# Performance work log

Measured on AMD Instinct MI355X. Metric: run time of the kernel, lower is better.

Reference implementation:

```python
import jax, jax.numpy as jnp
import numpy as np

B, T, H, W = 8, 10, 128, 128
WIDTH, NL = 64, 4
MT, MH, MW = 4, 8, 8
H_PRED = 5
MIN_STD = 1e-4


def setup_inputs() -> dict:
    key = jax.random.key(0)
    ks = jax.random.split(key, 12)
    scale = 1.0 / (WIDTH * WIDTH)
    return {
        "frames": jax.random.uniform(ks[0], (B, T, H, W), dtype=jnp.float32),
        "times": jax.random.uniform(ks[1], (B, T), dtype=jnp.float32),
        # lift: Conv3d(c_in=2 -> width, k=1)
        "lift_w": jax.random.normal(ks[2], (WIDTH, 2), dtype=jnp.float32) * 0.5,
        "lift_b": jnp.zeros((WIDTH,), jnp.float32),
        # spectral weights: (layer, quadrant, in, out, mt, mh, mw, re/im)
        "spec_w": jax.random.uniform(ks[3], (NL, 4, WIDTH, WIDTH, MT, MH, MW, 2), dtype=jnp.float32) * scale,
        # skip 1x1 Conv3d per layer
        "skip_w": jax.random.normal(ks[4], (NL, WIDTH, WIDTH), dtype=jnp.float32) * (1.0 / np.sqrt(WIDTH)),
        "skip_b": jnp.zeros((NL, WIDTH), jnp.float32),
        # temporal aggregation Conv3d kernel (h_ctx,1,1): (out, in, T)
        "agg_w": jax.random.normal(ks[5], (WIDTH, WIDTH, T), dtype=jnp.float32) * (1.0 / np.sqrt(WIDTH * T)),
        "agg_b": jnp.zeros((WIDTH,), jnp.float32),
        "fc1_w": jax.random.normal(ks[6], (WIDTH + 2, 128), dtype=jnp.float32) * (1.0 / np.sqrt(WIDTH + 2)),
        "fc1_b": jnp.zeros((128,), jnp.float32),
        "fc2_w": jax.random.normal(ks[7], (128, 2 * H_PRED), dtype=jnp.float32) * (1.0 / np.sqrt(128)),
        "fc2_b": jnp.zeros((2 * H_PRED,), jnp.float32),
    }


def _spectral_conv(x, wl):
    # x: (B, C, T, H, W); wl: (4, C, C, MT, MH, MW, 2) real/imag
    w = wl[..., 0] + 1j * wl[..., 1]  # (4, C, C, MT, MH, MW) complex
    x_ft = jnp.fft.rfftn(x, axes=(-3, -2, -1), norm="ortho")  # (B,C,T,H,W//2+1)
    Bc, C, Tt, Hh, Wf = x_ft.shape

    def mul(blk, wq):
        return jnp.einsum("bixyz,ioxyz->boxyz", blk, wq)

    out_ft = jnp.zeros((Bc, C, Tt, Hh, Wf), dtype=x_ft.dtype)
    out_ft = out_ft.at[:, :, :MT, :MH, :MW].set(mul(x_ft[:, :, :MT, :MH, :MW], w[0]))
    out_ft = out_ft.at[:, :, :MT, Hh - MH:, :MW].set(mul(x_ft[:, :, :MT, Hh - MH:, :MW], w[1]))
    out_ft = out_ft.at[:, :, Tt - MT:, :MH, :MW].set(mul(x_ft[:, :, Tt - MT:, :MH, :MW], w[2]))
    out_ft = out_ft.at[:, :, Tt - MT:, Hh - MH:, :MW].set(mul(x_ft[:, :, Tt - MT:, Hh - MH:, :MW], w[3]))
    return jnp.fft.irfftn(out_ft, s=(Tt, x.shape[-2], x.shape[-1]), axes=(-3, -2, -1), norm="ortho")


def reference(frames, times, lift_w, lift_b, spec_w, skip_w, skip_b,
              agg_w, agg_b, fc1_w, fc1_b, fc2_w, fc2_b):
    gelu = lambda v: jax.nn.gelu(v, approximate=False)
    # feature volume: (B, 2, T, H, W) = [frames, broadcast times]
    t_feat = jnp.broadcast_to(times[:, None, :, None, None], (B, 1, T, H, W))
    feat = jnp.concatenate([frames[:, None], t_feat], axis=1)
    # lift (1x1x1 conv)
    x = jnp.einsum("bcthw,oc->bothw", feat, lift_w) + lift_b[None, :, None, None, None]
    for l in range(NL):
        sx = _spectral_conv(x, spec_w[l])
        sk = jnp.einsum("bithw,oi->bothw", x, skip_w[l]) + skip_b[l][None, :, None, None, None]
        x = gelu(sx + sk)
    # temporal aggregation: valid conv over full T -> (B, C, H, W)
    x = jnp.einsum("bithw,oit->bohw", x, agg_w) + agg_b[None, :, None, None]
    # (x, y) grid channels
    gx = jnp.broadcast_to(jnp.linspace(-1.0, 1.0, W)[None, :], (H, W))
    gy = jnp.broadcast_to(jnp.linspace(-1.0, 1.0, H)[:, None], (H, W))
    grid = jnp.broadcast_to(jnp.stack([gx, gy], 0)[None], (B, 2, H, W))
    x = jnp.concatenate([x, grid], axis=1)  # (B, C+2, H, W)
    x = jnp.transpose(x, (0, 2, 3, 1))      # (B, H, W, C+2)
    x = gelu(x @ fc1_w + fc1_b)
    out = x @ fc2_w + fc2_b                 # (B, H, W, 2*h_pred)
    mu = out[..., 0::2]
    sigma = jax.nn.softplus(out[..., 1::2]) + MIN_STD
    return jnp.concatenate([mu, sigma], axis=-1)  # (B, H, W, 2*h_pred)
```

## Files before the change

kernel.cpp:

```cpp
#include <hip/hip_runtime.h>
#include <math.h>


#define TWO_PI 6.2831853071795864769f
#define ORTHO_SC 2.4705294220065465e-3f

typedef unsigned short u16;
typedef _Float16 f16;
typedef __attribute__((ext_vector_type(8))) _Float16 f16x8;
typedef __attribute__((ext_vector_type(4))) float f32x4;

#define MFMAH(acc, a, b) acc = __builtin_amdgcn_mfma_f32_16x16x32_f16(a, b, acc, 0, 0, 0)

__device__ __forceinline__ u16 f16b(float v) {
  f16 h = (f16)v;
  return __builtin_bit_cast(u16, h);
}
__device__ __forceinline__ float f16lo(float v) {
  f16 h = (f16)v;
  return v - (float)h;
}
__device__ __forceinline__ float f16f(u16 b) {
  return (float)__builtin_bit_cast(f16, b);
}
__device__ __forceinline__ float gelu_fast(float x) {
  float u = 0.7978845608f * (x + 0.044715f * x * x * x);
  float a = fminf(u * 2.885390082f, 30.0f);
  float e = __builtin_exp2f(a);
  return x * e * __builtin_amdgcn_rcpf(e + 1.0f);
}

__global__ __launch_bounds__(256) void k_prep2(const float* __restrict__ skip_w,
                                               const float* __restrict__ agg_w,
                                               u16* __restrict__ swf,
                                               u16* __restrict__ awf,
                                               u16* __restrict__ Tt,
                                               float2* __restrict__ twf,
                                               u16* __restrict__ Ef) {
  int e = blockIdx.x*256 + threadIdx.x;
  if (e < 32768) {
    int j = e & 7, lane = (e >> 3) & 63, half = (e >> 9) & 1, ks = (e >> 10) & 1;
    int strip = (e >> 11) & 3, layer = e >> 13;
    int co = strip*16 + (lane & 15);
    int ci = ks*32 + (lane >> 4)*8 + j;
    float v = skip_w[((size_t)(layer*64) + co)*64 + ci];
    swf[e] = half ? f16b(f16lo(v)) : f16b(v);
  } else if (e < 114688) {
    int ee = e - 32768;
    int j = ee & 7, lane = (ee >> 3) & 63;
    int v9 = ee >> 9;
    int half = v9 & 1; v9 >>= 1;
    int ks = v9 & 1; v9 >>= 1;
    int t = v9 % 10, strip = v9 / 10;
    int co = strip*16 + (lane & 15);
    int ci = ks*32 + (lane >> 4)*8 + j;
    float v = agg_w[((size_t)co*64 + ci)*10 + t];
    awf[ee] = half ? f16b(f16lo(v)) : f16b(v);
  } else if (e < 122880) {
    int ee = e - 114688;
    int half = ee >> 12, r = ee & 4095, w = r >> 5, kk = r & 31;
    int m = kk >> 1;
    float val;
    if (kk >= 16) val = 0.f;
    else if (kk == 0) val = 1.f;
    else if (kk == 1) val = 0.f;
    else {
      float th = TWO_PI * (float)m * (float)w / 128.0f;
      val = (kk & 1) ? (-2.f*sinf(th)) : (2.f*cosf(th));
    }
    Tt[ee] = half ? f16b(f16lo(val)) : f16b(val);
  } else if (e < 123904) {
    int ee = e - 122880;
    int w = ee >> 3, k = ee & 7;
    float th = TWO_PI * (float)k * (float)w / 128.0f;
    twf[ee] = make_float2(cosf(th), -sinf(th));
  } else if (e < 125952) {
    int ee = e - 123904;
    int j = ee & 7, lane = (ee >> 3) & 63, kc = ee >> 9;
    int n = lane & 15, g = lane >> 4;
    int w = kc*32 + g*8 + j;
    int k = n >> 1;
    float th = TWO_PI * (float)k * (float)w / 128.0f;
    float val = (n & 1) ? (-sinf(th)) : cosf(th);
    Ef[ee] = f16b(val);
    Ef[2048 + ee] = f16b(f16lo(val));
  }
}

__global__ __launch_bounds__(128) void k_lift_fwdW(const float* __restrict__ frames,
                                                   const float* __restrict__ times,
                                                   const float* __restrict__ lift_w,
                                                   const float* __restrict__ lift_b,
                                                   const float2* __restrict__ twf,
                                                   u16* __restrict__ xT,
                                                   float* __restrict__ xw) {
  __shared__ u16 xs[64][130];
  __shared__ float2 tws[128][8];
  __shared__ float fr[128];
  __shared__ float lw0[64], lw1a[64];
  int bth = blockIdx.x;
  int h = bth & 127; int bt = bth >> 7; int t = bt % 10, b = bt / 10;
  int tid = threadIdx.x;
  for (int i = tid; i < 1024; i += 128) tws[i >> 3][i & 7] = twf[i];
  float tv = times[b*10 + t];
  fr[tid] = frames[((size_t)(b*10 + t)*128 + h)*128 + tid];
  if (tid < 64) { lw0[tid] = lift_w[2*tid]; lw1a[tid] = lift_w[2*tid+1]*tv + lift_b[tid]; }
  __syncthreads();
  {
    int w = tid;
    float f = fr[w];
    unsigned pk[32];
    #pragma unroll
    for (int q = 0; q < 32; ++q) {
      float v0 = f*lw0[2*q] + lw1a[2*q];
      float v1 = f*lw0[2*q+1] + lw1a[2*q+1];
      u16 h0 = f16b(v0), h1 = f16b(v1);
      xs[2*q][w] = h0; xs[2*q+1][w] = h1;
      pk[q] = (unsigned)h0 | ((unsigned)h1 << 16);
    }
    uint4* d4 = (uint4*)(xT + (size_t)bth*8192 + w*64);
    #pragma unroll
    for (int q = 0; q < 8; ++q)
      d4[q] = make_uint4(pk[4*q], pk[4*q+1], pk[4*q+2], pk[4*q+3]);
  }
  __syncthreads();
  {
    int lane = tid & 63, wv = tid >> 6;
    float ar[4] = {0,0,0,0}, ai[4] = {0,0,0,0};
    for (int w2 = 0; w2 < 128; ++w2) {
      float xu = f16f(xs[lane][w2]);
      #pragma unroll
      for (int kk = 0; kk < 4; ++kk) {
        float2 ew = tws[w2][wv*4 + kk];
        ar[kk] += xu*ew.x; ai[kk] += xu*ew.y;
      }
    }
    size_t row = ((size_t)(b*64 + lane)*10 + t)*128 + h;
    float4* dst = (float4*)(xw + row*16 + wv*8);
    dst[0] = make_float4(ar[0], ai[0], ar[1], ai[1]);
    dst[1] = make_float4(ar[2], ai[2], ar[3], ai[3]);
  }
}

__global__ __launch_bounds__(256) void k_fwdHT(const float2* __restrict__ xw,
                                               float2* __restrict__ xf) {
  __shared__ float2 tile[2][1024];
  __shared__ float2 tw128[128];
  int bc = blockIdx.x;
  int b = bc >> 6, c = bc & 63;
  int tid = threadIdx.x;
  if (tid < 128) {
    float s, co; sincosf(TWO_PI * (float)tid / 128.0f, &s, &co);
    tw128[tid] = make_float2(co, -s);
  }
  int tpar = tid >> 7, j = tid & 127;
  int khi = j >> 3, kwi = j & 7;
  int kh = (khi < 8) ? khi : (112 + khi);
  float accr[8], acci[8];
  #pragma unroll
  for (int k = 0; k < 8; ++k) { accr[k] = 0.f; acci[k] = 0.f; }
  for (int tt = 0; tt < 5; ++tt) {
    __syncthreads();
    for (int u = tid; u < 2048; u += 256) {
      int tg = u >> 10, idx = u & 1023;
      tile[tg][idx] = xw[((size_t)bc*10 + tg*5 + tt)*1024 + idx];
    }
    __syncthreads();
    float xr = 0.f, xi = 0.f;
    for (int h = 0; h < 128; ++h) {
      float2 v = tile[tpar][h*8 + kwi];
      float2 tw = tw128[(h*kh) & 127];
      xr += v.x*tw.x - v.y*tw.y;
      xi += v.x*tw.y + v.y*tw.x;
    }
    int t = tpar*5 + tt;
    float sb, cb; sincosf(TWO_PI * (float)t / 10.0f, &sb, &cb);
    float p_r[10], p_i[10];
    p_r[0] = 1.f; p_i[0] = 0.f; p_r[1] = cb; p_i[1] = -sb;
    #pragma unroll
    for (int k = 2; k < 10; ++k) {
      p_r[k] = p_r[k-1]*p_r[1] - p_i[k-1]*p_i[1];
      p_i[k] = p_r[k-1]*p_i[1] + p_i[k-1]*p_r[1];
    }
    #pragma unroll
    for (int kti = 0; kti < 8; ++kti) {
      int kt = (kti < 4) ? kti : kti + 2;
      accr[kti] += xr*p_r[kt] - xi*p_i[kt];
      acci[kti] += xr*p_i[kt] + xi*p_r[kt];
    }
  }
  __syncthreads();
  float2* parts = &tile[0][0];
  #pragma unroll
  for (int kti = 0; kti < 8; ++kti)
    parts[tpar*1024 + j*8 + kti] = make_float2(accr[kti], acci[kti]);
  __syncthreads();
  if (tpar == 0) {
    #pragma unroll
    for (int kti = 0; kti < 8; ++kti) {
      float2 a = parts[j*8 + kti], bq = parts[1024 + j*8 + kti];
      xf[((size_t)b*1024 + kti*128 + j)*64 + c] =
          make_float2((a.x + bq.x)*ORTHO_SC, (a.y + bq.y)*ORTHO_SC);
    }
  }
}

__global__ __launch_bounds__(256) void k_prep_w4(const float* __restrict__ spec_w,
                                                 float2* __restrict__ wT4) {
  __shared__ float2 tile[64][65];
  int blk = blockIdx.x;
  int l = blk >> 10;
  int inner = blk & 1023;
  int mc = inner & 3, ci = (inner >> 2) & 63, q = inner >> 8;
  const float2* in = (const float2*)spec_w + (size_t)l*4194304
                     + (((size_t)q*64 + ci)*64)*256 + mc*64;
  for (int i = threadIdx.x; i < 4096; i += 256) {
    int co = i >> 6, mm = i & 63;
    tile[co][mm] = in[(size_t)co*256 + mm];
  }
  __syncthreads();
  float2* out = wT4 + (size_t)l*4194304 + ((size_t)q*256 + mc*64)*4096 + (size_t)ci*64;
  for (int i = threadIdx.x; i < 4096; i += 256) {
    int mm = i >> 6, co = i & 63;
    out[(size_t)mm*4096 + co] = tile[co][mm];
  }
}

__global__ __launch_bounds__(256) void k_mix(const float2* __restrict__ xf,
                                             const float2* __restrict__ wTl,
                                             float2* __restrict__ yf) {
  __shared__ float2 xfs[8][4][64];
  int m0 = blockIdx.x * 4;
  for (int i = threadIdx.x; i < 2048; i += 256) {
    int bb = i >> 8, mi = (i >> 6) & 3, ci = i & 63;
    xfs[bb][mi][ci] = xf[((size_t)bb*1024 + m0 + mi)*64 + ci];
  }
  __syncthreads();
  int co = threadIdx.x & 63, mi = threadIdx.x >> 6;
  int m = m0 + mi;
  int kti = m >> 7, khi = (m >> 3) & 15, kwi = m & 7;
  int q = ((kti >= 4) ? 2 : 0) + ((khi >= 8) ? 1 : 0);
  int modeidx = ((kti & 3)*8 + (khi & 7))*8 + kwi;
  const float2* wp = wTl + ((size_t)q*256 + modeidx)*4096 + co;
  float accr[8], acci[8];
  #pragma unroll
  for (int bb = 0; bb < 8; ++bb) { accr[bb] = 0.f; acci[bb] = 0.f; }
  for (int ci = 0; ci < 64; ++ci) {
    float2 wv = wp[(size_t)ci*64];
    #pragma unroll
    for (int bb = 0; bb < 8; ++bb) {
      float2 xv = xfs[bb][mi][ci];
      accr[bb] += xv.x*wv.x - xv.y*wv.y;
      acci[bb] += xv.x*wv.y + xv.y*wv.x;
    }
  }
  #pragma unroll
  for (int bb = 0; bb < 8; ++bb)
    yf[((size_t)bb*64 + co)*1024 + m] = make_float2(accr[bb], acci[bb]);
}

__global__ __launch_bounds__(256) void k_invTH(const float2* __restrict__ yf,
                                               unsigned* __restrict__ zh16) {
  __shared__ float2 ybuf[1024];
  __shared__ float2 ztb[2][128];
  __shared__ float2 tw128[128];
  int bc = blockIdx.x;
  int b = bc >> 6, c = bc & 63;
  int tid = threadIdx.x;
  for (int u = tid; u < 1024; u += 256) ybuf[u] = yf[(size_t)bc*1024 + u];
  if (tid < 128) {
    float s, co; sincosf(TWO_PI * (float)tid / 128.0f, &s, &co);
    tw128[tid] = make_float2(co, s);
  }
  int tpar = tid >> 7, j = tid & 127;
  __syncthreads();
  for (int tt = 0; tt < 5; ++tt) {
    int t = tt*2 + tpar;
    {
      float sb, cb; sincosf(TWO_PI * (float)t / 10.0f, &sb, &cb);
      float p_r[10], p_i[10];
      p_r[0] = 1.f; p_i[0] = 0.f; p_r[1] = cb; p_i[1] = sb;
      #pragma unroll
      for (int k = 2; k < 10; ++k) {
        p_r[k] = p_r[k-1]*p_r[1] - p_i[k-1]*p_i[1];
        p_i[k] = p_r[k-1]*p_i[1] + p_i[k-1]*p_r[1];
      }
      float zr = 0.f, zi = 0.f;
      #pragma unroll
      for (int kti = 0; kti < 8; ++kti) {
        int kt = (kti < 4) ? kti : kti + 2;
        float2 v = ybuf[kti*128 + j];
        zr += v.x*p_r[kt] - v.y*p_i[kt];
        zi += v.x*p_i[kt] + v.y*p_r[kt];
      }
      ztb[tpar][j] = make_float2(zr*ORTHO_SC, zi*ORTHO_SC);
    }
    __syncthreads();
    {
      int h = j;
      float ar[8], ai[8];
      #pragma unroll
      for (int kw = 0; kw < 8; ++kw) { ar[kw] = 0.f; ai[kw] = 0.f; }
      #pragma unroll
      for (int khi = 0; khi < 16; ++khi) {
        int kh = (khi < 8) ? khi : (112 + khi);
        float2 tw = tw128[(h*kh) & 127];
        #pragma unroll
        for (int kw = 0; kw < 8; ++kw) {
          float2 v = ztb[tpar][khi*8 + kw];
          ar[kw] += v.x*tw.x - v.y*tw.y;
          ai[kw] += v.x*tw.y + v.y*tw.x;
        }
      }
      unsigned* dst = zh16 + (((size_t)(b*10 + t)*128 + h)*64 + c)*8;
      #pragma unroll
      for (int kw = 0; kw < 8; ++kw)
        dst[kw] = (unsigned)f16b(ar[kw]) | ((unsigned)f16b(ai[kw]) << 16);
    }
    __syncthreads();
  }
}

__global__ __launch_bounds__(256) void k_invW_mfma(const u16* __restrict__ xTin,
                                                   const unsigned* __restrict__ zh16,
                                                   const u16* __restrict__ swf_l,
                                                   const u16* __restrict__ Tt,
                                                   const u16* __restrict__ Ef,
                                                   const float* __restrict__ skb,
                                                   u16* __restrict__ xTo,
                                                   float* __restrict__ xw,
                                                   int do_dft) {
  __shared__ __align__(16) char smem[36864];
  u16* B = (u16*)smem;
  u16* zAh = (u16*)(smem + 34816);
  int tid = threadIdx.x;
  int bth = blockIdx.x;
  {
    const uint4* xsrc = (const uint4*)(xTin + (size_t)bth*8192);
    for (int u = tid; u < 1024; u += 256) {
      int w = u >> 3, c = u & 7;
      ((uint4*)(B + w*136))[c] = xsrc[u];
    }
  }
  if (tid < 256) {
    int w = tid >> 1, half = tid & 1;
    const uint4* sh = (const uint4*)(Tt + w*32 + half*16);
    const uint4* sl = (const uint4*)(Tt + 4096 + w*32 + half*16);
    uint4* dh = (uint4*)(B + w*136 + 64 + half*16);
    uint4* dl = (uint4*)(B + w*136 + 96 + half*16);
    dh[0] = sh[0]; dh[1] = sh[1];
    dl[0] = sl[0]; dl[1] = sl[1];
  }
  {
    const unsigned* zsrc = zh16 + (size_t)bth*512;
    for (int u = tid; u < 512; u += 256) {
      int co = u >> 3, m = u & 7;
      *(unsigned*)(zAh + co*16 + 2*m) = zsrc[u];
    }
  }
  __syncthreads();

  int lane = tid & 63;
  int wq = tid >> 6;
  int cL = lane & 15;
  int g = lane >> 4;

  f32x4 acc[4][2];
  #pragma unroll
  for (int s = 0; s < 4; ++s)
    #pragma unroll
    for (int t2 = 0; t2 < 2; ++t2) acc[s][t2] = (f32x4){0.f,0.f,0.f,0.f};

  #pragma unroll
  for (int kb = 0; kb < 2; ++kb) {
    f16x8 Ah[4], Al[4];
    #pragma unroll
    for (int s = 0; s < 4; ++s) {
      Ah[s] = *(const f16x8*)(swf_l + (size_t)(s*2048 + kb*1024 + lane*8));
      Al[s] = *(const f16x8*)(swf_l + (size_t)(s*2048 + kb*1024 + 512 + lane*8));
    }
    #pragma unroll
    for (int t2 = 0; t2 < 2; ++t2) {
      int wrow = wq*32 + t2*16 + cL;
      f16x8 bh = *(const f16x8*)(B + wrow*136 + kb*32 + g*8);
      #pragma unroll
      for (int s = 0; s < 4; ++s) {
        MFMAH(acc[s][t2], Ah[s], bh);
        MFMAH(acc[s][t2], Al[s], bh);
      }
    }
  }
  {
    f16x8 Azh[4];
    f16x8 zero8 = {0,0,0,0,0,0,0,0};
    #pragma unroll
    for (int s = 0; s < 4; ++s)
      Azh[s] = (g < 2) ? *(const f16x8*)(zAh + (s*16 + cL)*16 + g*8) : zero8;
    #pragma unroll
    for (int t2 = 0; t2 < 2; ++t2) {
      int wrow = wq*32 + t2*16 + cL;
      f16x8 th = *(const f16x8*)(B + wrow*136 + 64 + g*8);
      f16x8 tl = *(const f16x8*)(B + wrow*136 + 96 + g*8);
      #pragma unroll
      for (int s = 0; s < 4; ++s) {
        MFMAH(acc[s][t2], Azh[s], th);
        MFMAH(acc[s][t2], Azh[s], tl);
      }
    }
  }

  __syncthreads();
  unsigned* out32 = (unsigned*)smem;
  u16* xg_a = (u16*)(smem + 16512);
  #pragma unroll
  for (int s = 0; s < 4; ++s) {
    float4 b4 = *(const float4*)(skb + s*16 + g*4);
    float bb[4] = {b4.x, b4.y, b4.z, b4.w};
    #pragma unroll
    for (int t2 = 0; t2 < 2; ++t2) {
      int w = wq*32 + t2*16 + cL;
      float ge[4];
      u16 gb[4];
      #pragma unroll
      for (int r = 0; r < 4; ++r) {
        float val = acc[s][t2][r] + bb[r];
        ge[r] = gelu_fast(val);
        gb[r] = f16b(ge[r]);
      }
      out32[(s*8 + g*2 + 0)*129 + w] = (unsigned)gb[0] | ((unsigned)gb[1] << 16);
      out32[(s*8 + g*2 + 1)*129 + w] = (unsigned)gb[2] | ((unsigned)gb[3] << 16);
      if (do_dft) {
        #pragma unroll
        for (int r = 0; r < 4; ++r)
          xg_a[(s*16 + g*4 + r)*136 + w] = gb[r];
      }
    }
  }
  __syncthreads();
  {
    uint4* xdst = (uint4*)(xTo + (size_t)bth*8192);
    for (int u = tid; u < 1024; u += 256) {
      int w = u >> 3, c = u & 7;
      unsigned r0 = out32[(c*4 + 0)*129 + w];
      unsigned r1 = out32[(c*4 + 1)*129 + w];
      unsigned r2 = out32[(c*4 + 2)*129 + w];
      unsigned r3 = out32[(c*4 + 3)*129 + w];
      xdst[u] = make_uint4(r0, r1, r2, r3);
    }
  }
  if (do_dft) {
    f32x4 acc2 = (f32x4){0.f,0.f,0.f,0.f};
    #pragma unroll
    for (int kc = 0; kc < 4; ++kc) {
      f16x8 a = *(const f16x8*)(xg_a + (wq*16 + cL)*136 + kc*32 + g*8);
      f16x8 eh = *(const f16x8*)(Ef + (kc*64 + lane)*8);
      f16x8 el = *(const f16x8*)(Ef + 2048 + (kc*64 + lane)*8);
      MFMAH(acc2, a, eh);
      MFMAH(acc2, a, el);
    }
    int h = bth & 127; int bt = bth >> 7; int t = bt % 10, b = bt / 10;
    #pragma unroll
    for (int r = 0; r < 4; ++r) {
      int co = wq*16 + g*4 + r;
      size_t row = ((size_t)(b*64 + co)*10 + t)*128 + h;
      xw[row*16 + cL] = acc2[r];
    }
  }
}

__global__ __launch_bounds__(256) void k_agg_mfma(const u16* __restrict__ xT,
                                                  const u16* __restrict__ awf,
                                                  const float* __restrict__ agg_b,
                                                  float* __restrict__ xa) {
  __shared__ __align__(16) char smem[36864];
  u16* B = (u16*)smem;
  int tid = threadIdx.x;
  int bid = blockIdx.x;
  int h = bid & 127, b = bid >> 7;
  int lane = tid & 63;
  int wq = tid >> 6;
  int cL = lane & 15;
  int g = lane >> 4;

  f32x4 acc[4][2];
  #pragma unroll
  for (int s = 0; s < 4; ++s)
    #pragma unroll
    for (int t2 = 0; t2 < 2; ++t2) acc[s][t2] = (f32x4){0.f,0.f,0.f,0.f};

  for (int t = 0; t < 10; ++t) {
    __syncthreads();
    {
      const uint4* xsrc = (const uint4*)(xT + ((size_t)(b*10 + t)*128 + h)*8192);
      for (int u = tid; u < 1024; u += 256) {
        int w = u >> 3, c = u & 7;
        ((uint4*)(B + w*72))[c] = xsrc[u];
      }
    }
    __syncthreads();
    #pragma unroll
    for (int kc = 0; kc < 2; ++kc) {
      f16x8 Ah[4], Al[4];
      #pragma unroll
      for (int s = 0; s < 4; ++s) {
        const u16* af = awf + (size_t)((s*10 + t)*4 + kc*2)*512;
        Ah[s] = *(const f16x8*)(af + lane*8);
        Al[s] = *(const f16x8*)(af + 512 + lane*8);
      }
      #pragma unroll
      for (int t2 = 0; t2 < 2; ++t2) {
        int wrow = wq*32 + t2*16 + cL;
        f16x8 bh = *(const f16x8*)(B + wrow*72 + kc*32 + g*8);
        #pragma unroll
        for (int s = 0; s < 4; ++s) {
          MFMAH(acc[s][t2], Ah[s], bh);
          MFMAH(acc[s][t2], Al[s], bh);
        }
      }
    }
  }

  __syncthreads();
  float* outT = (float*)smem;
  #pragma unroll
  for (int s = 0; s < 4; ++s) {
    float4 b4 = *(const float4*)(agg_b + s*16 + g*4);
    float bb[4] = {b4.x, b4.y, b4.z, b4.w};
    #pragma unroll
    for (int t2 = 0; t2 < 2; ++t2) {
      int w = wq*32 + t2*16 + cL;
      #pragma unroll
      for (int r = 0; r < 4; ++r) {
        int co = s*16 + g*4 + r;
        outT[co*132 + w] = acc[s][t2][r] + bb[r];
      }
    }
  }
  __syncthreads();
  for (int u = tid; u < 256; u += 256) {
    int co = u >> 2, c32 = u & 3;
    float* dst = xa + ((size_t)(b*64 + co)*128 + h)*128 + c32*32;
    #pragma unroll
    for (int q = 0; q < 8; ++q) {
      float4 vv = make_float4(outT[co*132 + c32*32 + 4*q],
                              outT[co*132 + c32*32 + 4*q + 1],
                              outT[co*132 + c32*32 + 4*q + 2],
                              outT[co*132 + c32*32 + 4*q + 3]);
      ((float4*)dst)[q] = vv;
    }
  }
}

__global__ __launch_bounds__(128) void k_head(const float* __restrict__ xa,
                                              const float* __restrict__ fc1_w,
                                              const float* __restrict__ fc1_b,
                                              const float* __restrict__ fc2_w,
                                              const float* __restrict__ fc2_b,
                                              float* __restrict__ out) {
  __shared__ float w1[66*128];
  __shared__ float w2[128*10];
  __shared__ float b1s[128];
  __shared__ float b2s[16];
  int bid = blockIdx.x;
  int h = bid & 127, b = bid >> 7;
  int tid = threadIdx.x;
  for (int i = tid; i < 66*128; i += 128) w1[i] = fc1_w[i];
  for (int i = tid; i < 1280; i += 128) w2[i] = fc2_w[i];
  b1s[tid] = fc1_b[tid];
  if (tid < 10) b2s[tid] = fc2_b[tid];
  float v[64];
  #pragma unroll
  for (int c = 0; c < 64; ++c)
    v[c] = xa[((size_t)(b*64 + c)*128 + h)*128 + tid];
  __syncthreads();
  float gx = -1.f + 2.f*(float)tid/127.f;
  float gy = -1.f + 2.f*(float)h/127.f;
  float o2[10];
  #pragma unroll
  for (int j = 0; j < 10; ++j) o2[j] = b2s[j];
  for (int o = 0; o < 128; ++o) {
    float a = b1s[o];
    #pragma unroll
    for (int i = 0; i < 64; ++i) a += v[i]*w1[i*128 + o];
    a += gx*w1[64*128 + o] + gy*w1[65*128 + o];
    float g = gelu_fast(a);
    #pragma unroll
    for (int j = 0; j < 10; ++j) o2[j] += g*w2[o*10 + j];
  }
  float* dst = out + ((size_t)bid*128 + tid)*10;
  #pragma unroll
  for (int k = 0; k < 5; ++k) dst[k] = o2[2*k];
  #pragma unroll
  for (int k = 0; k < 5; ++k) {
    float sv = o2[2*k+1];
    float sp = fmaxf(sv, 0.f) + log1pf(expf(-fabsf(sv)));
    dst[5 + k] = sp + 1e-4f;
  }
}

extern "C" void kernel_launch(void* const* d_in, const int* in_sizes, int n_in,
                              void* d_out, int out_size, void* d_ws, size_t ws_size,
                              hipStream_t stream) {
  const float* frames = (const float*)d_in[0];
  const float* times  = (const float*)d_in[1];
  const float* lift_w = (const float*)d_in[2];
  const float* lift_b = (const float*)d_in[3];
  const float* spec_w = (const float*)d_in[4];
  const float* skip_w = (const float*)d_in[5];
  const float* skip_b = (const float*)d_in[6];
  const float* agg_w  = (const float*)d_in[7];
  const float* agg_b  = (const float*)d_in[8];
  const float* fc1_w  = (const float*)d_in[9];
  const float* fc1_b  = (const float*)d_in[10];
  const float* fc2_w  = (const float*)d_in[11];
  const float* fc2_b  = (const float*)d_in[12];
  float* out = (float*)d_out;
  char* ws = (char*)d_ws;

  size_t off = 0;
  u16*      xT  = (u16*)(ws + off);      off += (size_t)10240*8192*2;
  float*    xw  = (float*)(ws + off);    off += (size_t)655360*16*4;
  float2*   xf  = (float2*)(ws + off);   off += (size_t)8*1024*64*8;
  float2*   yf  = (float2*)(ws + off);   off += (size_t)8*1024*64*8;
  unsigned* zh16= (unsigned*)(ws + off); off += (size_t)10240*512*4;
  float*    xa  = (float*)(ws + off);    off += (size_t)8*64*128*128*4;
  float2*   wT4 = (float2*)(ws + off);   off += (size_t)4*4194304*8;
  u16*      swf = (u16*)(ws + off);      off += (size_t)32768*2;
  u16*      awf = (u16*)(ws + off);      off += (size_t)81920*2;
  u16*      Tt  = (u16*)(ws + off);      off += (size_t)8192*2;
  float2*   twf = (float2*)(ws + off);   off += (size_t)1024*8;
  u16*      Ef  = (u16*)(ws + off);      off += (size_t)4096*2;

  k_prep2<<<492, 256, 0, stream>>>(skip_w, agg_w, swf, awf, Tt, twf, Ef);
  k_prep_w4<<<4096, 256, 0, stream>>>(spec_w, wT4);
  k_lift_fwdW<<<10240, 128, 0, stream>>>(frames, times, lift_w, lift_b, twf, xT, xw);

  for (int l = 0; l < 4; ++l) {
    k_fwdHT<<<512, 256, 0, stream>>>((const float2*)xw, xf);
    k_mix<<<256, 256, 0, stream>>>(xf, wT4 + (size_t)l*4194304, yf);
    k_invTH<<<512, 256, 0, stream>>>(yf, zh16);
    k_invW_mfma<<<10240, 256, 0, stream>>>(xT, zh16, swf + (size_t)l*8192, Tt, Ef,
                                           skip_b + l*64, xT, xw, (l < 3) ? 1 : 0);
  }
  k_agg_mfma<<<1024, 256, 0, stream>>>(xT, awf, agg_b, xa);
  k_head<<<1024, 128, 0, stream>>>(xa, fc1_w, fc1_b, fc2_w, fc2_b, out);
}
```

Baseline: 1.127 ms.

## Shrink LDS in inverse-W and aggregation kernels to raise occupancy

The inverse-W kernel no longer stages the twiddle table in LDS. Each lane loads its own T fragments straight from global memory into registers, and the DFT operand is read back from the packed output buffer instead of a separate xg_a copy. Together these cut shared memory from 36 KB to 20 KB, and the launch bounds now request 6 blocks per CU. The aggregation kernel drops its LDS transpose and writes results directly to global memory, which makes those stores less coalesced. These changes trade extra global loads, unpacking work and possible register pressure for higher occupancy and fewer barriers.

```diff
diff --git a/kernel.cpp b/kernel.cpp
--- a/kernel.cpp
+++ b/kernel.cpp
@@ -321,35 +321,38 @@
   }
 }
 
-__global__ __launch_bounds__(256) void k_invW_mfma(const u16* __restrict__ xTin,
-                                                   const unsigned* __restrict__ zh16,
-                                                   const u16* __restrict__ swf_l,
-                                                   const u16* __restrict__ Tt,
-                                                   const u16* __restrict__ Ef,
-                                                   const float* __restrict__ skb,
-                                                   u16* __restrict__ xTo,
-                                                   float* __restrict__ xw,
-                                                   int do_dft) {
-  __shared__ __align__(16) char smem[36864];
+__global__ __launch_bounds__(256, 6) void k_invW_mfma(const u16* __restrict__ xTin,
+                                                      const unsigned* __restrict__ zh16,
+                                                      const u16* __restrict__ swf_l,
+                                                      const u16* __restrict__ Tt,
+                                                      const u16* __restrict__ Ef,
+                                                      const float* __restrict__ skb,
+                                                      u16* __restrict__ xTo,
+                                                      float* __restrict__ xw,
+                                                      int do_dft) {
+  __shared__ __align__(16) char smem[20480];
   u16* B = (u16*)smem;
-  u16* zAh = (u16*)(smem + 34816);
+  u16* zAh = (u16*)(smem + 18432);
   int tid = threadIdx.x;
   int bth = blockIdx.x;
+  int lane = tid & 63;
+  int wq = tid >> 6;
+  int cL = lane & 15;
+  int g = lane >> 4;
+
+  f16x8 Th[2], Tl[2];
+  #pragma unroll
+  for (int t2 = 0; t2 < 2; ++t2) {
+    int wrow = wq*32 + t2*16 + cL;
+    Th[t2] = *(const f16x8*)(Tt + wrow*32 + g*8);
+    Tl[t2] = *(const f16x8*)(Tt + 4096 + wrow*32 + g*8);
+  }
   {
     const uint4* xsrc = (const uint4*)(xTin + (size_t)bth*8192);
     for (int u = tid; u < 1024; u += 256) {
       int w = u >> 3, c = u & 7;
-      ((uint4*)(B + w*136))[c] = xsrc[u];
-    }
-  }
-  if (tid < 256) {
-    int w = tid >> 1, half = tid & 1;
-    const uint4* sh = (const uint4*)(Tt + w*32 + half*16);
-    const uint4* sl = (const uint4*)(Tt + 4096 + w*32 + half*16);
-    uint4* dh = (uint4*)(B + w*136 + 64 + half*16);
-    uint4* dl = (uint4*)(B + w*136 + 96 + half*16);
-    dh[0] = sh[0]; dh[1] = sh[1];
-    dl[0] = sl[0]; dl[1] = sl[1];
+      ((uint4*)(B + w*72))[c] = xsrc[u];
+    }
   }
   {
     const unsigned* zsrc = zh16 + (size_t)bth*512;
@@ -360,11 +363,6 @@
   }
   __syncthreads();
 
-  int lane = tid & 63;
-  int wq = tid >> 6;
-  int cL = lane & 15;
-  int g = lane >> 4;
-
   f32x4 acc[4][2];
   #pragma unroll
   for (int s = 0; s < 4; ++s)
@@ -382,7 +380,7 @@
     #pragma unroll
     for (int t2 = 0; t2 < 2; ++t2) {
       int wrow = wq*32 + t2*16 + cL;
-      f16x8 bh = *(const f16x8*)(B + wrow*136 + kb*32 + g*8);
+      f16x8 bh = *(const f16x8*)(B + wrow*72 + kb*32 + g*8);
       #pragma unroll
       for (int s = 0; s < 4; ++s) {
         MFMAH(acc[s][t2], Ah[s], bh);
@@ -398,20 +396,16 @@
       Azh[s] = (g < 2) ? *(const f16x8*)(zAh + (s*16 + cL)*16 + g*8) : zero8;
     #pragma unroll
     for (int t2 = 0; t2 < 2; ++t2) {
-      int wrow = wq*32 + t2*16 + cL;
-      f16x8 th = *(const f16x8*)(B + wrow*136 + 64 + g*8);
-      f16x8 tl = *(const f16x8*)(B + wrow*136 + 96 + g*8);
       #pragma unroll
       for (int s = 0; s < 4; ++s) {
-        MFMAH(acc[s][t2], Azh[s], th);
-        MFMAH(acc[s][t2], Azh[s], tl);
+        MFMAH(acc[s][t2], Azh[s], Th[t2]);
+        MFMAH(acc[s][t2], Azh[s], Tl[t2]);
       }
     }
   }
 
   __syncthreads();
   unsigned* out32 = (unsigned*)smem;
-  u16* xg_a = (u16*)(smem + 16512);
   #pragma unroll
   for (int s = 0; s < 4; ++s) {
     float4 b4 = *(const float4*)(skb + s*16 + g*4);
@@ -419,21 +413,14 @@
     #pragma unroll
     for (int t2 = 0; t2 < 2; ++t2) {
       int w = wq*32 + t2*16 + cL;
-      float ge[4];
       u16 gb[4];
       #pragma unroll
       for (int r = 0; r < 4; ++r) {
         float val = acc[s][t2][r] + bb[r];
-        ge[r] = gelu_fast(val);
-        gb[r] = f16b(ge[r]);
-      }
-      out32[(s*8 + g*2 + 0)*129 + w] = (unsigned)gb[0] | ((unsigned)gb[1] << 16);
-      out32[(s*8 + g*2 + 1)*129 + w] = (unsigned)gb[2] | ((unsigned)gb[3] << 16);
-      if (do_dft) {
-        #pragma unroll
-        for (int r = 0; r < 4; ++r)
-          xg_a[(s*16 + g*4 + r)*136 + w] = gb[r];
-      }
+        gb[r] = f16b(gelu_fast(val));
+      }
+      out32[(s*8 + g*2 + 0)*130 + w] = (unsigned)gb[0] | ((unsigned)gb[1] << 16);
+      out32[(s*8 + g*2 + 1)*130 + w] = (unsigned)gb[2] | ((unsigned)gb[3] << 16);
     }
   }
   __syncthreads();
@@ -441,18 +428,33 @@
     uint4* xdst = (uint4*)(xTo + (size_t)bth*8192);
     for (int u = tid; u < 1024; u += 256) {
       int w = u >> 3, c = u & 7;
-      unsigned r0 = out32[(c*4 + 0)*129 + w];
-      unsigned r1 = out32[(c*4 + 1)*129 + w];
-      unsigned r2 = out32[(c*4 + 2)*129 + w];
-      unsigned r3 = out32[(c*4 + 3)*129 + w];
+      unsigned r0 = out32[(c*4 + 0)*130 + w];
+      unsigned r1 = out32[(c*4 + 1)*130 + w];
+      unsigned r2 = out32[(c*4 + 2)*130 + w];
+      unsigned r3 = out32[(c*4 + 3)*130 + w];
       xdst[u] = make_uint4(r0, r1, r2, r3);
     }
   }
   if (do_dft) {
     f32x4 acc2 = (f32x4){0.f,0.f,0.f,0.f};
+    int row = wq*8 + (cL >> 1);
+    int sh = (cL & 1) * 16;
     #pragma unroll
     for (int kc = 0; kc < 4; ++kc) {
-      f16x8 a = *(const f16x8*)(xg_a + (wq*16 + cL)*136 + kc*32 + g*8);
+      const unsigned* p = out32 + row*130 + kc*32 + g*8;
+      uint2 d0 = *(const uint2*)(p);
+      uint2 d1 = *(const uint2*)(p + 2);
+      uint2 d2 = *(const uint2*)(p + 4);
+      uint2 d3 = *(const uint2*)(p + 6);
+      f16x8 a;
+      a[0] = __builtin_bit_cast(f16, (u16)(d0.x >> sh));
+      a[1] = __builtin_bit_cast(f16, (u16)(d0.y >> sh));
+      a[2] = __builtin_bit_cast(f16, (u16)(d1.x >> sh));
+      a[3] = __builtin_bit_cast(f16, (u16)(d1.y >> sh));
+      a[4] = __builtin_bit_cast(f16, (u16)(d2.x >> sh));
+      a[5] = __builtin_bit_cast(f16, (u16)(d2.y >> sh));
+      a[6] = __builtin_bit_cast(f16, (u16)(d3.x >> sh));
+      a[7] = __builtin_bit_cast(f16, (u16)(d3.y >> sh));
       f16x8 eh = *(const f16x8*)(Ef + (kc*64 + lane)*8);
       f16x8 el = *(const f16x8*)(Ef + 2048 + (kc*64 + lane)*8);
       MFMAH(acc2, a, eh);
@@ -462,8 +464,8 @@
     #pragma unroll
     for (int r = 0; r < 4; ++r) {
       int co = wq*16 + g*4 + r;
-      size_t row = ((size_t)(b*64 + co)*10 + t)*128 + h;
-      xw[row*16 + cL] = acc2[r];
+      size_t row2 = ((size_t)(b*64 + co)*10 + t)*128 + h;
+      xw[row2*16 + cL] = acc2[r];
     }
   }
 }
@@ -472,8 +474,7 @@
                                                   const u16* __restrict__ awf,
                                                   const float* __restrict__ agg_b,
                                                   float* __restrict__ xa) {
-  __shared__ __align__(16) char smem[36864];
-  u16* B = (u16*)smem;
+  __shared__ __align__(16) u16 B[128*72];
   int tid = threadIdx.x;
   int bid = blockIdx.x;
   int h = bid & 127, b = bid >> 7;
@@ -520,8 +521,6 @@
     }
   }
 
-  __syncthreads();
-  float* outT = (float*)smem;
   #pragma unroll
   for (int s = 0; s < 4; ++s) {
     float4 b4 = *(const float4*)(agg_b + s*16 + g*4);
@@ -532,21 +531,8 @@
       #pragma unroll
       for (int r = 0; r < 4; ++r) {
         int co = s*16 + g*4 + r;
-        outT[co*132 + w] = acc[s][t2][r] + bb[r];
-      }
-    }
-  }
-  __syncthreads();
-  for (int u = tid; u < 256; u += 256) {
-    int co = u >> 2, c32 = u & 3;
-    float* dst = xa + ((size_t)(b*64 + co)*128 + h)*128 + c32*32;
-    #pragma unroll
-    for (int q = 0; q < 8; ++q) {
-      float4 vv = make_float4(outT[co*132 + c32*32 + 4*q],
-                              outT[co*132 + c32*32 + 4*q + 1],
-                              outT[co*132 + c32*32 + 4*q + 2],
-                              outT[co*132 + c32*32 + 4*q + 3]);
-      ((float4*)dst)[q] = vv;
+        xa[((size_t)(b*64 + co)*128 + h)*128 + w] = acc[s][t2][r] + bb[r];
+      }
     }
   }
 }
```

Result: slower. 1.290 ms (+14.5%).
